# Kernel optimization log

Hardware: AMD Instinct MI355X
Metric: run time of the kernel (lower is better)

Reference implementation:

```python
import jax, jax.numpy as jnp
import numpy as np
import math

B, S, D, H = 4, 2048, 1024, 16
DK = D // H


def setup_inputs() -> dict:
    key = jax.random.key(0)
    ks = jax.random.split(key, 11)
    s = 1.0 / math.sqrt(D)
    inp = {
        "query": jax.random.normal(ks[0], (B, S, D), jnp.float32),
        "key": jax.random.normal(ks[1], (B, S, D), jnp.float32),
        "value": jax.random.normal(ks[2], (B, S, D), jnp.float32),
        # torch nn.Linear params: weight [out,in], bias [out]
        "Wq": jax.random.uniform(ks[3], (D, D), jnp.float32, -s, s),
        "bq": jax.random.uniform(ks[4], (D,), jnp.float32, -s, s),
        "Wk": jax.random.uniform(ks[5], (D, D), jnp.float32, -s, s),
        "bk": jax.random.uniform(ks[6], (D,), jnp.float32, -s, s),
        "Wv": jax.random.uniform(ks[7], (D, D), jnp.float32, -s, s),
        "bv": jax.random.uniform(ks[8], (D,), jnp.float32, -s, s),
        "Wo": jax.random.uniform(ks[9], (D, D), jnp.float32, -s, s),
        "bo": jax.random.uniform(ks[10], (D,), jnp.float32, -s, s),
    }
    return inp


def _split_heads(x):
    # [B,S,D] -> [B,H,S,DK]
    return x.reshape(B, S, H, DK).transpose(0, 2, 1, 3)


def reference(query, key, value, Wq, bq, Wk, bk, Wv, bv, Wo, bo):
    q = _split_heads(query @ Wq.T + bq)
    k = _split_heads(key @ Wk.T + bk)
    v = _split_heads(value @ Wv.T + bv)
    scores = jnp.einsum("bhqd,bhkd->bhqk", q, k) / math.sqrt(DK)
    p = jax.nn.softmax(scores, axis=-1)  # dropout p=0 -> identity
    x = jnp.einsum("bhqk,bhkd->bhqd", p, v)
    x = x.transpose(0, 2, 1, 3).reshape(B, S, D)
    return x @ Wo.T + bo
```

## Files before the change

### kernel.cpp

```cpp
#include <hip/hip_runtime.h>
#include <hip/hip_bf16.h>


typedef __attribute__((ext_vector_type(8))) short bf16x8;
typedef __attribute__((ext_vector_type(4))) float f32x4;

static __device__ __forceinline__ unsigned short f2bf(float f) {
  union { __hip_bfloat16 h; unsigned short u; } cv;
  cv.h = __float2bfloat16(f);
  return cv.u;
}

static __device__ __forceinline__ unsigned int pack2bf(float a, float b) {
  union { __hip_bfloat162 h; unsigned int u; } cv;
  cv.h = __float22bfloat162_rn(float2{a, b});
  return cv.u;
}

static __device__ __forceinline__ void gload_lds16(const void* g, void* l) {
  __builtin_amdgcn_global_load_lds(
      (const __attribute__((address_space(1))) unsigned int*)g,
      (__attribute__((address_space(3))) unsigned int*)l, 16, 0, 0);
}

__global__ __launch_bounds__(256) void cvt_kernel(const float* __restrict__ in,
                                                  unsigned short* __restrict__ out,
                                                  int n) {
  int i = (blockIdx.x * 256 + threadIdx.x) * 4;
  if (i + 3 < n) {
    float4 v = *(const float4*)(in + i);
    ushort4 o;
    o.x = f2bf(v.x); o.y = f2bf(v.y); o.z = f2bf(v.z); o.w = f2bf(v.w);
    *(ushort4*)(out + i) = o;
  }
}

template<int MODE>
__global__ __launch_bounds__(256) void gemm_bt(const unsigned short* __restrict__ A,
                                               const unsigned short* __restrict__ Bw,
                                               const float* __restrict__ bias,
                                               void* __restrict__ outp,
                                               int M, int N, int K) {
  __shared__ unsigned short As[128 * 32];
  __shared__ unsigned short Bs[128 * 32];
  const int tid = threadIdx.x;
  const int w = tid >> 6, lane = tid & 63;
  const int wr = w >> 1, wc = w & 1;
  const int fr = lane & 15, fg = lane >> 4;

  int bx, by;
  if (MODE != 2) {
    const int nwg = gridDim.x * gridDim.y;
    const int lin = blockIdx.y * gridDim.x + blockIdx.x;
    const int nb = (lin & 7) * (nwg >> 3) + (lin >> 3);
    bx = nb % gridDim.x; by = nb / gridDim.x;
  } else {
    bx = blockIdx.x; by = blockIdx.y;
  }
  const int m0 = by * 128, n0 = bx * 128;

  f32x4 acc[4][4] = {};
  const int e0 = (w * 2) * 512 + lane * 8;

  for (int kt = 0; kt < K; kt += 32) {
#pragma unroll
    for (int i = 0; i < 2; ++i) {
      const int e = e0 + i * 512;
      const int row = e >> 5, kk = e & 31;
      gload_lds16(A + (size_t)(m0 + row) * K + kt + kk, (void*)(As + e));
      gload_lds16(Bw + (size_t)(n0 + row) * K + kt + kk, (void*)(Bs + e));
    }
    __syncthreads();
    bf16x8 af[4], bfr[4];
#pragma unroll
    for (int m = 0; m < 4; ++m)
      af[m] = *(const bf16x8*)(As + (wr * 64 + m * 16 + fr) * 32 + fg * 8);
#pragma unroll
    for (int n = 0; n < 4; ++n)
      bfr[n] = *(const bf16x8*)(Bs + (wc * 64 + n * 16 + fr) * 32 + fg * 8);
#pragma unroll
    for (int m = 0; m < 4; ++m)
#pragma unroll
      for (int n = 0; n < 4; ++n)
        acc[m][n] = __builtin_amdgcn_mfma_f32_16x16x32_bf16(af[m], bfr[n], acc[m][n], 0, 0, 0);
    __syncthreads();
  }

#pragma unroll
  for (int m = 0; m < 4; ++m) {
#pragma unroll
    for (int n = 0; n < 4; ++n) {
      const int gn = n0 + wc * 64 + n * 16 + fr;
#pragma unroll
      for (int r = 0; r < 4; ++r) {
        const int gm = m0 + wr * 64 + m * 16 + fg * 4 + r;
        float val = acc[m][n][r];
        if (MODE == 2) val += bias[gm]; else val += bias[gn];
        if (MODE == 0) {
          val *= 0.125f;
          size_t idx = ((size_t)((gm >> 11) * 16 + (gn >> 6)) * 2048 + (gm & 2047)) * 64 + (gn & 63);
          ((unsigned short*)outp)[idx] = f2bf(val);
        } else if (MODE == 1) {
          size_t idx = ((size_t)((gm >> 11) * 16 + (gn >> 6)) * 2048 + (gm & 2047)) * 64 + (gn & 63);
          ((unsigned short*)outp)[idx] = f2bf(val);
        } else if (MODE == 2) {
          size_t idx = ((size_t)((gn >> 11) * 16 + (gm >> 6)) * 64 + (gm & 63)) * 2048 + (gn & 2047);
          ((unsigned short*)outp)[idx] = f2bf(val);
        } else {
          ((float*)outp)[(size_t)gm * N + gn] = val;
        }
      }
    }
  }
}

__global__ __launch_bounds__(256, 2) void attn_kernel(const unsigned short* __restrict__ Qh,
                                                      const unsigned short* __restrict__ Kh,
                                                      const unsigned short* __restrict__ Vt,
                                                      unsigned short* __restrict__ Xa) {
  const int S = 2048, DK = 64;
  __shared__ unsigned short Psm[4][64 * 72];
  __shared__ float Ssum[4][64];
  const int tid = threadIdx.x;
  const int w = tid >> 6, lane = tid & 63;
  const int fr = lane & 15, fg = lane >> 4;

  const int bid = blockIdx.x;
  const int xcd = bid & 7, slot = bid >> 3;
  const int bh = xcd * 8 + (slot >> 3);
  const int qblk = slot & 7;
  const int q0 = qblk * 256 + w * 64;

  const unsigned short* Qp = Qh + (size_t)bh * S * DK;
  const unsigned short* Kp = Kh + (size_t)bh * S * DK;
  const unsigned short* Vp = Vt + (size_t)bh * DK * S;
  unsigned short* Pw = Psm[w];

  bf16x8 qf[4][2];
#pragma unroll
  for (int nt = 0; nt < 4; ++nt)
#pragma unroll
    for (int ks = 0; ks < 2; ++ks)
      qf[nt][ks] = *(const bf16x8*)(Qp + (size_t)(q0 + nt * 16 + fr) * DK + ks * 32 + fg * 8);

  f32x4 xacc[4][4] = {};
  float psum[4] = {0.f, 0.f, 0.f, 0.f};

  for (int kv = 0; kv < S; kv += 64) {
    bf16x8 kf[4][2];
#pragma unroll
    for (int mt = 0; mt < 4; ++mt)
#pragma unroll
      for (int ks = 0; ks < 2; ++ks)
        kf[mt][ks] = *(const bf16x8*)(Kp + (size_t)(kv + mt * 16 + fr) * DK + ks * 32 + fg * 8);
    bf16x8 vf[4][2];
#pragma unroll
    for (int dn = 0; dn < 4; ++dn)
#pragma unroll
      for (int ks = 0; ks < 2; ++ks)
        vf[dn][ks] = *(const bf16x8*)(Vp + (size_t)(dn * 16 + fr) * S + kv + ks * 32 + fg * 8);

#pragma unroll
    for (int mt = 0; mt < 4; ++mt) {
      f32x4 sc[4];
#pragma unroll
      for (int nt = 0; nt < 4; ++nt) {
        sc[nt] = (f32x4){0.f, 0.f, 0.f, 0.f};
#pragma unroll
        for (int ks = 0; ks < 2; ++ks)
          sc[nt] = __builtin_amdgcn_mfma_f32_16x16x32_bf16(kf[mt][ks], qf[nt][ks], sc[nt], 0, 0, 0);
      }
#pragma unroll
      for (int nt = 0; nt < 4; ++nt) {
        const float p0 = __expf(sc[nt][0]);
        const float p1 = __expf(sc[nt][1]);
        const float p2 = __expf(sc[nt][2]);
        const float p3 = __expf(sc[nt][3]);
        psum[nt] += (p0 + p1) + (p2 + p3);
        *(uint2*)(Pw + (nt * 16 + fr) * 72 + mt * 16 + fg * 4) =
            make_uint2(pack2bf(p0, p1), pack2bf(p2, p3));
      }
    }

#pragma unroll
    for (int ks = 0; ks < 2; ++ks) {
      bf16x8 pf[4];
#pragma unroll
      for (int m = 0; m < 4; ++m)
        pf[m] = *(const bf16x8*)(Pw + (m * 16 + fr) * 72 + ks * 32 + fg * 8);
#pragma unroll
      for (int m = 0; m < 4; ++m)
#pragma unroll
        for (int dn = 0; dn < 4; ++dn)
          xacc[m][dn] = __builtin_amdgcn_mfma_f32_16x16x32_bf16(pf[m], vf[dn][ks], xacc[m][dn], 0, 0, 0);
    }
  }

#pragma unroll
  for (int nt = 0; nt < 4; ++nt) {
    psum[nt] += __shfl_xor(psum[nt], 16);
    psum[nt] += __shfl_xor(psum[nt], 32);
  }
  if (lane < 16) {
#pragma unroll
    for (int nt = 0; nt < 4; ++nt) Ssum[w][nt * 16 + lane] = psum[nt];
  }

  const int b = bh >> 4, h = bh & 15;
#pragma unroll
  for (int m = 0; m < 4; ++m) {
#pragma unroll
    for (int r = 0; r < 4; ++r) {
      const float inv = 1.f / Ssum[w][m * 16 + fg * 4 + r];
      const int s = q0 + m * 16 + fg * 4 + r;
      unsigned short* dst = Xa + ((size_t)(b * 2048 + s)) * 1024 + h * 64;
#pragma unroll
      for (int dn = 0; dn < 4; ++dn)
        dst[dn * 16 + fr] = f2bf(xacc[m][dn][r] * inv);
    }
  }
}

extern "C" void kernel_launch(void* const* d_in, const int* in_sizes, int n_in,
                              void* d_out, int out_size, void* d_ws, size_t ws_size,
                              hipStream_t stream) {
  (void)in_sizes; (void)n_in; (void)out_size;
  const float* q  = (const float*)d_in[0];
  const float* k  = (const float*)d_in[1];
  const float* v  = (const float*)d_in[2];
  const float* Wq = (const float*)d_in[3];
  const float* bq = (const float*)d_in[4];
  const float* Wk = (const float*)d_in[5];
  const float* bk = (const float*)d_in[6];
  const float* Wv = (const float*)d_in[7];
  const float* bv = (const float*)d_in[8];
  const float* Wo = (const float*)d_in[9];
  const float* bo = (const float*)d_in[10];
  float* out = (float*)d_out;

  const size_t XB = (size_t)8192 * 1024;
  const size_t WB = (size_t)1024 * 1024;
  const size_t need = (7 * XB + 4 * WB) * 2;
  if (ws_size < need) return;

  unsigned short* ws  = (unsigned short*)d_ws;
  unsigned short* xq  = ws;
  unsigned short* xk  = xq + XB;
  unsigned short* xv  = xk + XB;
  unsigned short* wqb = xv + XB;
  unsigned short* wkb = wqb + WB;
  unsigned short* wvb = wkb + WB;
  unsigned short* wob = wvb + WB;
  unsigned short* Qh  = wob + WB;
  unsigned short* Kh  = Qh + XB;
  unsigned short* Vt  = Kh + XB;
  unsigned short* Xa  = Vt + XB;

  cvt_kernel<<<XB / 1024, 256, 0, stream>>>(q, xq, (int)XB);
  cvt_kernel<<<XB / 1024, 256, 0, stream>>>(k, xk, (int)XB);
  cvt_kernel<<<XB / 1024, 256, 0, stream>>>(v, xv, (int)XB);
  cvt_kernel<<<WB / 1024, 256, 0, stream>>>(Wq, wqb, (int)WB);
  cvt_kernel<<<WB / 1024, 256, 0, stream>>>(Wk, wkb, (int)WB);
  cvt_kernel<<<WB / 1024, 256, 0, stream>>>(Wv, wvb, (int)WB);
  cvt_kernel<<<WB / 1024, 256, 0, stream>>>(Wo, wob, (int)WB);

  dim3 gMN(8, 64);
  dim3 gNM(64, 8);
  gemm_bt<0><<<gMN, 256, 0, stream>>>(xq, wqb, bq, Qh, 8192, 1024, 1024);
  gemm_bt<1><<<gMN, 256, 0, stream>>>(xk, wkb, bk, Kh, 8192, 1024, 1024);
  gemm_bt<2><<<gNM, 256, 0, stream>>>(wvb, xv, bv, Vt, 1024, 8192, 1024);

  attn_kernel<<<dim3(512), 256, 0, stream>>>(Qh, Kh, Vt, Xa);

  gemm_bt<3><<<gMN, 256, 0, stream>>>(Xa, wob, bo, out, 8192, 1024, 1024);
}
```

Before: 412.3 us.

## Keep attention probabilities in registers via permlane swaps; batch conversion and Q/K GEMM launches

The attention kernel no longer writes the bf16 probability tile to LDS and reads it back for the PV product. It reorders the score loop per query tile and uses v_permlane32/16 swaps to turn the MFMA output layout into the A-operand layout directly in registers. Separately, the seven fp32-to-bf16 conversion launches become two batched launches, and the Q and K projection GEMMs are merged into one launch using blockIdx.z. This cuts LDS traffic and launch overhead, but relies on the permlane lane mapping being correct and on the layout of contiguous workspace buffers.

Measured after the change: 393.7 us. 4.5% less time.

```diff
diff --git a/kernel.cpp b/kernel.cpp
--- a/kernel.cpp
+++ b/kernel.cpp
@@ -17,17 +17,28 @@
   return cv.u;
 }
 
+static __device__ __forceinline__ void pl32swap(unsigned int& a, unsigned int& b) {
+  asm volatile("v_permlane32_swap_b32 %0, %1" : "+v"(a), "+v"(b));
+}
+static __device__ __forceinline__ void pl16swap(unsigned int& a, unsigned int& b) {
+  asm volatile("v_permlane16_swap_b32 %0, %1" : "+v"(a), "+v"(b));
+}
+
 static __device__ __forceinline__ void gload_lds16(const void* g, void* l) {
   __builtin_amdgcn_global_load_lds(
       (const __attribute__((address_space(1))) unsigned int*)g,
       (__attribute__((address_space(3))) unsigned int*)l, 16, 0, 0);
 }
 
-__global__ __launch_bounds__(256) void cvt_kernel(const float* __restrict__ in,
-                                                  unsigned short* __restrict__ out,
-                                                  int n) {
+template<int NJ>
+struct CvtJobs { const float* in[NJ]; unsigned short* out[NJ]; int n; };
+
+template<int NJ>
+__global__ __launch_bounds__(256) void cvt_batch(CvtJobs<NJ> jobs) {
+  const float* __restrict__ in = jobs.in[blockIdx.y];
+  unsigned short* __restrict__ out = jobs.out[blockIdx.y];
   int i = (blockIdx.x * 256 + threadIdx.x) * 4;
-  if (i + 3 < n) {
+  if (i + 3 < jobs.n) {
     float4 v = *(const float4*)(in + i);
     ushort4 o;
     o.x = f2bf(v.x); o.y = f2bf(v.y); o.z = f2bf(v.z); o.w = f2bf(v.w);
@@ -36,9 +47,10 @@
 }
 
 template<int MODE>
-__global__ __launch_bounds__(256) void gemm_bt(const unsigned short* __restrict__ A,
-                                               const unsigned short* __restrict__ Bw,
+__global__ __launch_bounds__(256) void gemm_bt(const unsigned short* __restrict__ A_,
+                                               const unsigned short* __restrict__ Bw_,
                                                const float* __restrict__ bias,
+                                               const float* __restrict__ bias1,
                                                void* __restrict__ outp,
                                                int M, int N, int K) {
   __shared__ unsigned short As[128 * 32];
@@ -48,6 +60,18 @@
   const int wr = w >> 1, wc = w & 1;
   const int fr = lane & 15, fg = lane >> 4;
 
+  const unsigned short* A = A_;
+  const unsigned short* Bw = Bw_;
+  float scale = 1.f;
+  unsigned short* out16 = (unsigned short*)outp;
+  if (MODE == 4) {
+    const int z = blockIdx.z;
+    A += (size_t)z * (8192 * 1024);
+    Bw += (size_t)z * (1024 * 1024);
+    out16 += (size_t)z * (8192 * 1024);
+    if (z == 0) scale = 0.125f; else bias = bias1;
+  }
+
   int bx, by;
   if (MODE != 2) {
     const int nwg = gridDim.x * gridDim.y;
@@ -96,16 +120,13 @@
         const int gm = m0 + wr * 64 + m * 16 + fg * 4 + r;
         float val = acc[m][n][r];
         if (MODE == 2) val += bias[gm]; else val += bias[gn];
-        if (MODE == 0) {
-          val *= 0.125f;
+        if (MODE == 4) {
+          val *= scale;
           size_t idx = ((size_t)((gm >> 11) * 16 + (gn >> 6)) * 2048 + (gm & 2047)) * 64 + (gn & 63);
-          ((unsigned short*)outp)[idx] = f2bf(val);
-        } else if (MODE == 1) {
-          size_t idx = ((size_t)((gm >> 11) * 16 + (gn >> 6)) * 2048 + (gm & 2047)) * 64 + (gn & 63);
-          ((unsigned short*)outp)[idx] = f2bf(val);
+          out16[idx] = f2bf(val);
         } else if (MODE == 2) {
           size_t idx = ((size_t)((gn >> 11) * 16 + (gm >> 6)) * 64 + (gm & 63)) * 2048 + (gn & 2047);
-          ((unsigned short*)outp)[idx] = f2bf(val);
+          out16[idx] = f2bf(val);
         } else {
           ((float*)outp)[(size_t)gm * N + gn] = val;
         }
@@ -119,7 +140,6 @@
                                                       const unsigned short* __restrict__ Vt,
                                                       unsigned short* __restrict__ Xa) {
   const int S = 2048, DK = 64;
-  __shared__ unsigned short Psm[4][64 * 72];
   __shared__ float Ssum[4][64];
   const int tid = threadIdx.x;
   const int w = tid >> 6, lane = tid & 63;
@@ -134,7 +154,6 @@
   const unsigned short* Qp = Qh + (size_t)bh * S * DK;
   const unsigned short* Kp = Kh + (size_t)bh * S * DK;
   const unsigned short* Vp = Vt + (size_t)bh * DK * S;
-  unsigned short* Pw = Psm[w];
 
   bf16x8 qf[4][2];
 #pragma unroll
@@ -161,38 +180,46 @@
         vf[dn][ks] = *(const bf16x8*)(Vp + (size_t)(dn * 16 + fr) * S + kv + ks * 32 + fg * 8);
 
 #pragma unroll
-    for (int mt = 0; mt < 4; ++mt) {
+    for (int nt = 0; nt < 4; ++nt) {
       f32x4 sc[4];
 #pragma unroll
-      for (int nt = 0; nt < 4; ++nt) {
-        sc[nt] = (f32x4){0.f, 0.f, 0.f, 0.f};
-#pragma unroll
-        for (int ks = 0; ks < 2; ++ks)
-          sc[nt] = __builtin_amdgcn_mfma_f32_16x16x32_bf16(kf[mt][ks], qf[nt][ks], sc[nt], 0, 0, 0);
-      }
-#pragma unroll
-      for (int nt = 0; nt < 4; ++nt) {
-        const float p0 = __expf(sc[nt][0]);
-        const float p1 = __expf(sc[nt][1]);
-        const float p2 = __expf(sc[nt][2]);
-        const float p3 = __expf(sc[nt][3]);
-        psum[nt] += (p0 + p1) + (p2 + p3);
-        *(uint2*)(Pw + (nt * 16 + fr) * 72 + mt * 16 + fg * 4) =
-            make_uint2(pack2bf(p0, p1), pack2bf(p2, p3));
-      }
-    }
-
-#pragma unroll
-    for (int ks = 0; ks < 2; ++ks) {
-      bf16x8 pf[4];
-#pragma unroll
-      for (int m = 0; m < 4; ++m)
-        pf[m] = *(const bf16x8*)(Pw + (m * 16 + fr) * 72 + ks * 32 + fg * 8);
-#pragma unroll
-      for (int m = 0; m < 4; ++m)
-#pragma unroll
-        for (int dn = 0; dn < 4; ++dn)
-          xacc[m][dn] = __builtin_amdgcn_mfma_f32_16x16x32_bf16(pf[m], vf[dn][ks], xacc[m][dn], 0, 0, 0);
+      for (int mt = 0; mt < 4; ++mt) {
+        sc[mt] = __builtin_amdgcn_mfma_f32_16x16x32_bf16(kf[mt][0], qf[nt][0],
+                                                         (f32x4){0.f, 0.f, 0.f, 0.f}, 0, 0, 0);
+        sc[mt] = __builtin_amdgcn_mfma_f32_16x16x32_bf16(kf[mt][1], qf[nt][1], sc[mt], 0, 0, 0);
+      }
+      unsigned int X[4][2];
+      float ps = 0.f;
+#pragma unroll
+      for (int mt = 0; mt < 4; ++mt) {
+        const float p0 = __expf(sc[mt][0]);
+        const float p1 = __expf(sc[mt][1]);
+        const float p2 = __expf(sc[mt][2]);
+        const float p3 = __expf(sc[mt][3]);
+        ps += (p0 + p1) + (p2 + p3);
+        X[mt][0] = pack2bf(p0, p1);
+        X[mt][1] = pack2bf(p2, p3);
+      }
+      psum[nt] += ps;
+
+      union { unsigned int u[4]; bf16x8 b; } pa0, pa1;
+      {
+        unsigned int F0 = X[0][0], G0 = X[1][0]; pl32swap(F0, G0); pl16swap(F0, G0);
+        unsigned int F1 = X[0][1], G1 = X[1][1]; pl32swap(F1, G1); pl16swap(F1, G1);
+        pa0.u[0] = F0; pa0.u[1] = F1; pa0.u[2] = G0; pa0.u[3] = G1;
+      }
+      {
+        unsigned int F0 = X[2][0], G0 = X[3][0]; pl32swap(F0, G0); pl16swap(F0, G0);
+        unsigned int F1 = X[2][1], G1 = X[3][1]; pl32swap(F1, G1); pl16swap(F1, G1);
+        pa1.u[0] = F0; pa1.u[1] = F1; pa1.u[2] = G0; pa1.u[3] = G1;
+      }
+
+#pragma unroll
+      for (int dn = 0; dn < 4; ++dn)
+        xacc[nt][dn] = __builtin_amdgcn_mfma_f32_16x16x32_bf16(pa0.b, vf[dn][0], xacc[nt][dn], 0, 0, 0);
+#pragma unroll
+      for (int dn = 0; dn < 4; ++dn)
+        xacc[nt][dn] = __builtin_amdgcn_mfma_f32_16x16x32_bf16(pa1.b, vf[dn][1], xacc[nt][dn], 0, 0, 0);
     }
   }
 
@@ -256,21 +283,17 @@
   unsigned short* Vt  = Kh + XB;
   unsigned short* Xa  = Vt + XB;
 
-  cvt_kernel<<<XB / 1024, 256, 0, stream>>>(q, xq, (int)XB);
-  cvt_kernel<<<XB / 1024, 256, 0, stream>>>(k, xk, (int)XB);
-  cvt_kernel<<<XB / 1024, 256, 0, stream>>>(v, xv, (int)XB);
-  cvt_kernel<<<WB / 1024, 256, 0, stream>>>(Wq, wqb, (int)WB);
-  cvt_kernel<<<WB / 1024, 256, 0, stream>>>(Wk, wkb, (int)WB);
-  cvt_kernel<<<WB / 1024, 256, 0, stream>>>(Wv, wvb, (int)WB);
-  cvt_kernel<<<WB / 1024, 256, 0, stream>>>(Wo, wob, (int)WB);
-
-  dim3 gMN(8, 64);
-  dim3 gNM(64, 8);
-  gemm_bt<0><<<gMN, 256, 0, stream>>>(xq, wqb, bq, Qh, 8192, 1024, 1024);
-  gemm_bt<1><<<gMN, 256, 0, stream>>>(xk, wkb, bk, Kh, 8192, 1024, 1024);
-  gemm_bt<2><<<gNM, 256, 0, stream>>>(wvb, xv, bv, Vt, 1024, 8192, 1024);
+  CvtJobs<3> jx; jx.in[0] = q; jx.in[1] = k; jx.in[2] = v;
+  jx.out[0] = xq; jx.out[1] = xk; jx.out[2] = xv; jx.n = (int)XB;
+  cvt_batch<3><<<dim3(XB / 1024, 3), 256, 0, stream>>>(jx);
+  CvtJobs<4> jw; jw.in[0] = Wq; jw.in[1] = Wk; jw.in[2] = Wv; jw.in[3] = Wo;
+  jw.out[0] = wqb; jw.out[1] = wkb; jw.out[2] = wvb; jw.out[3] = wob; jw.n = (int)WB;
+  cvt_batch<4><<<dim3(WB / 1024, 4), 256, 0, stream>>>(jw);
+
+  gemm_bt<4><<<dim3(8, 64, 2), 256, 0, stream>>>(xq, wqb, bq, bk, Qh, 8192, 1024, 1024);
+  gemm_bt<2><<<dim3(64, 8), 256, 0, stream>>>(wvb, xv, bv, nullptr, Vt, 1024, 8192, 1024);
 
   attn_kernel<<<dim3(512), 256, 0, stream>>>(Qh, Kh, Vt, Xa);
 
-  gemm_bt<3><<<gMN, 256, 0, stream>>>(Xa, wob, bo, out, 8192, 1024, 1024);
-}
+  gemm_bt<3><<<dim3(8, 64), 256, 0, stream>>>(Xa, wob, bo, nullptr, out, 8192, 1024, 1024);
+}
```
